# Performance work log

Hardware: AMD Instinct MI355X
Metric: run time of the kernel (lower is better)

Reference implementation:

```python
import jax, jax.numpy as jnp
import numpy as np

V = 780        # junction-tree vocab size
N = 50000      # total nodes in batch
M = 100001     # total messages (+1 null slot at index 0)
K = 6          # padded max neighbors
H = 256        # hidden size
B = 64         # number of trees (scope entries)
DEPTH = 6      # GRU depth


def setup_inputs() -> dict:
    key = jax.random.key(0)
    ks = jax.random.split(key, 12)
    p = lambda k, s: jax.random.normal(k, s, jnp.float32) * 0.02
    return {
        "fnode": jax.random.randint(ks[0], (N,), 0, V),
        "fmess": jax.random.randint(ks[1], (M,), 0, N),
        "node_graph": jax.random.randint(ks[2], (N, K), 0, M),
        "mess_graph": jax.random.randint(ks[3], (M, K), 0, M),
        "scope_st": jax.random.randint(ks[4], (B,), 0, N),
        "emb": p(ks[5], (V, H)),
        "Wz": p(ks[6], (H, 2 * H)), "bz": jnp.zeros((H,), jnp.float32),
        "Wr": p(ks[7], (H, H)),
        "Ur": p(ks[8], (H, H)), "bu": jnp.zeros((H,), jnp.float32),
        "Wh": p(ks[9], (H, 2 * H)), "bh": jnp.zeros((H,), jnp.float32),
        "Wo": p(ks[10], (H, 2 * H)), "bo": jnp.zeros((H,), jnp.float32),
    }


def reference(fnode, fmess, node_graph, mess_graph, scope_st,
              emb, Wz, bz, Wr, Ur, bu, Wh, bh, Wo, bo):
    fnode_e = emb[fnode]                       # [N, H] embedded node features
    x = fnode_e[fmess]                         # [M, H] per-message source features
    mask = jnp.ones((M, 1), jnp.float32).at[0].set(0.0)  # zero the null message
    # W_r(x) depends only on x; hoist it out of the loop (same math as original)
    xWr = (x @ Wr.T)[:, None, :]               # [M, 1, H]

    h = jnp.zeros((M, H), jnp.float32)
    for _ in range(DEPTH):
        h_nei = h[mess_graph]                  # [M, K, H] gather neighbor messages
        sum_h = h_nei.sum(axis=1)              # [M, H]
        z = jax.nn.sigmoid(jnp.concatenate([x, sum_h], axis=1) @ Wz.T + bz)
        r = jax.nn.sigmoid(xWr + h_nei @ Ur.T + bu)   # [M, K, H]
        sum_gated_h = (r * h_nei).sum(axis=1)  # [M, H]
        pre_h = jnp.tanh(jnp.concatenate([x, sum_gated_h], axis=1) @ Wh.T + bh)
        h = ((1.0 - z) * sum_h + z * pre_h) * mask

    mess_nei = h[node_graph].sum(axis=1)       # [N, H]
    node_vecs = jax.nn.relu(
        jnp.concatenate([fnode_e, mess_nei], axis=-1) @ Wo.T + bo)  # [N, H]
    tree_vecs = node_vecs[scope_st]            # [B, H] root vector per tree
    return tree_vecs, h
```

## Files before the change

### kernel.cpp

```cpp
#include <hip/hip_runtime.h>

typedef unsigned short u16;
typedef unsigned int   u32;
typedef short bf16x8 __attribute__((ext_vector_type(8)));
typedef float f32x4  __attribute__((ext_vector_type(4)));

#define V_ 780
#define N_ 50000
#define M_ 100001
#define K_ 6
#define H_ 256
#define B_ 64
#define DEPTH_ 6

#define HE_LD 512

typedef __attribute__((address_space(3))) u32 lds_u32;
typedef __attribute__((address_space(1))) const u32 glb_u32;
__device__ __forceinline__ void dma16(const void* g, void* l){
  __builtin_amdgcn_global_load_lds((glb_u32*)g, (lds_u32*)l, 16, 0, 0);
}

__device__ __forceinline__ float b2f(u16 u){
  union { u32 i; float f; } x; x.i = ((u32)u) << 16; return x.f;
}
__device__ __forceinline__ u16 f2b(float f){
  union { float f; u32 i; } x; x.f = f;
  u32 r = x.i + 0x7fffu + ((x.i >> 16) & 1u);
  return (u16)(r >> 16);
}
__device__ __forceinline__ float rcp_(float x){ return __builtin_amdgcn_rcpf(x); }
__device__ __forceinline__ float sigm(float x){ return rcp_(1.f + __expf(-x)); }
__device__ __forceinline__ float tanh_(float x){
  x = fminf(fmaxf(x, -15.f), 15.f);
  float e = __expf(2.f*x);
  return (e - 1.f) * rcp_(e + 1.f);
}
__device__ __forceinline__ int swz(int r){ return (r + (r >> 2)) & 3; }

__global__ void k_tables(const float* __restrict__ emb,
    const float* __restrict__ Wz, const float* __restrict__ bz,
    const float* __restrict__ Wr, const float* __restrict__ bu,
    const float* __restrict__ Wh, const float* __restrict__ bh,
    const float* __restrict__ Wo, const float* __restrict__ bo,
    float* __restrict__ tWz, float* __restrict__ tXr,
    float* __restrict__ tWh, float* __restrict__ tWo){
  int v = blockIdx.x, q = blockIdx.y, j = threadIdx.x;
  __shared__ float e[H_];
  e[j] = emb[v*H_ + j];
  __syncthreads();
  const float* w; const float* b; float* o; int ld;
  if      (q == 0){ w = Wz; b = bz; o = tWz; ld = 2*H_; }
  else if (q == 1){ w = Wr; b = bu; o = tXr; ld = H_;   }
  else if (q == 2){ w = Wh; b = bh; o = tWh; ld = 2*H_; }
  else            { w = Wo; b = bo; o = tWo; ld = 2*H_; }
  const float* wr = w + (size_t)j*ld;
  float a0 = 0.f, a1 = 0.f;
  #pragma unroll 4
  for (int i = 0; i < H_; i += 8){
    float4 x = *(const float4*)(wr + i);
    float4 y = *(const float4*)(wr + i + 4);
    a0 += e[i  ]*x.x + e[i+1]*x.y + e[i+2]*x.z + e[i+3]*x.w;
    a1 += e[i+4]*y.x + e[i+5]*y.y + e[i+6]*y.z + e[i+7]*y.w;
  }
  float val = a0 + a1 + b[j];
  if (q == 1) val = __expf(-val);
  o[v*H_ + j] = val;
}

__global__ void k_convw(const float* __restrict__ Ur, const float* __restrict__ Wz,
                        const float* __restrict__ Wh,
                        u16* __restrict__ Urb, u16* __restrict__ Wzb, u16* __restrict__ Whb){
  int r = blockIdx.x, j = threadIdx.x;
  Urb[r*H_ + j] = f2b(Ur[r*H_ + j]);
  Wzb[r*H_ + j] = f2b(Wz[r*(2*H_) + H_ + j]);
  Whb[r*H_ + j] = f2b(Wh[r*(2*H_) + H_ + j]);
}

__global__ void k_init(const int* __restrict__ fnode, const int* __restrict__ fmess,
                       const float* __restrict__ tWz, const float* __restrict__ tWh,
                       int* __restrict__ vmsg, u16* __restrict__ hE){
  int m = blockIdx.x, j = threadIdx.x;
  int v = fnode[fmess[m]];
  if (j == 0) vmsg[m] = v;
  float val = (m == 0) ? 0.f : sigm(tWz[v*H_ + j])*tanh_(tWh[v*H_ + j]);
  hE[(size_t)m*HE_LD + j] = f2b(val);
}

__global__ void k_gather(const u16* __restrict__ hE,
                         const int* __restrict__ mg, const int* __restrict__ vmsg,
                         const float* __restrict__ tXr,
                         u16* __restrict__ sumh, u16* __restrict__ sumg){
  int m = blockIdx.x*4 + (threadIdx.x >> 6);
  if (m >= M_) return;
  const int lane = threadIdx.x & 63;
  int v = vmsg[m];
  float4 X = *(const float4*)(tXr + (size_t)v*H_ + lane*4);
  const int2* mgp = (const int2*)(mg + m*K_);
  int2 g01 = mgp[0], g23 = mgp[1], g45 = mgp[2];
  int gs[K_] = {g01.x, g01.y, g23.x, g23.y, g45.x, g45.y};
  const char* bc = (const char*)hE;
  const u32 cb = (u32)lane * 8u;
  float s0=0.f,s1=0.f,s2=0.f,s3=0.f, a0=0.f,a1=0.f,a2=0.f,a3=0.f;
  #pragma unroll
  for (int k=0;k<K_;k++){
    u32 off = ((u32)gs[k] << 10) + cb;
    uint2 hp = *(const uint2*)(bc + off);
    uint2 ep = *(const uint2*)(bc + off + 512);
    float h0=b2f((u16)hp.x), h1=b2f((u16)(hp.x>>16));
    float h2=b2f((u16)hp.y), h3=b2f((u16)(hp.y>>16));
    float e0=b2f((u16)ep.x), e1=b2f((u16)(ep.x>>16));
    float e2=b2f((u16)ep.y), e3=b2f((u16)(ep.y>>16));
    s0+=h0; s1+=h1; s2+=h2; s3+=h3;
    a0 += rcp_(fmaf(X.x,e0,1.f))*h0;
    a1 += rcp_(fmaf(X.y,e1,1.f))*h1;
    a2 += rcp_(fmaf(X.z,e2,1.f))*h2;
    a3 += rcp_(fmaf(X.w,e3,1.f))*h3;
  }
  uint2 sh, sg;
  sh.x = (u32)f2b(s0) | ((u32)f2b(s1)<<16);
  sh.y = (u32)f2b(s2) | ((u32)f2b(s3)<<16);
  sg.x = (u32)f2b(a0) | ((u32)f2b(a1)<<16);
  sg.y = (u32)f2b(a2) | ((u32)f2b(a3)<<16);
  *(uint2*)((char*)sumh + ((size_t)m<<9) + cb) = sh;
  *(uint2*)((char*)sumg + ((size_t)m<<9) + cb) = sg;
}

__global__ __launch_bounds__(512,4) void k_gemmE(
    const u16* hE, const u16* __restrict__ W){
  __shared__ __align__(16) u16 lA[128*32];
  __shared__ __align__(16) u16 lB[256*32];
  const int t    = threadIdx.x;
  const int m0   = blockIdx.x * 128;
  const int lane = t & 63, wave = t >> 6;
  const int wrow = wave >> 2, wcol = wave & 3;
  const int l16  = lane & 15, kc8 = lane >> 4;

  const int rA = t >> 2, cA = t & 3;
  const int kA = (cA ^ swz(rA)) * 8;
  const int gmA = (m0 + rA < M_) ? (m0 + rA) : (M_ - 1);
  u16* const dA = lA + (size_t)(wave*64)*8;
  int rB[2], kB[2];
  u16* dB[2];
  #pragma unroll
  for (int p=0;p<2;p++){
    int s = t + 512*p;
    rB[p] = s >> 2; int cB = s & 3;
    kB[p] = (cB ^ swz(rB[p])) * 8;
    dB[p] = lB + (size_t)(wave*64 + 512*p)*8;
  }

  f32x4 acc[4][4];
  #pragma unroll
  for (int r=0;r<4;r++)
    #pragma unroll
    for (int c=0;c<4;c++)
      #pragma unroll
      for (int q=0;q<4;q++) acc[r][c][q] = 0.f;

  for (int k0=0; k0<H_; k0+=32){
    __syncthreads();
    dma16(hE + (size_t)gmA*HE_LD + k0 + kA, dA);
    #pragma unroll
    for (int p=0;p<2;p++)
      dma16(W + (size_t)rB[p]*H_ + k0 + kB[p], dB[p]);
    __syncthreads();
    bf16x8 aF[4], bF[4];
    #pragma unroll
    for (int r=0;r<4;r++){
      int row = wrow*64 + r*16 + l16;
      aF[r] = *(const bf16x8*)(&lA[row*32 + ((kc8 ^ swz(row))*8)]);
    }
    #pragma unroll
    for (int c=0;c<4;c++){
      int row = wcol*64 + c*16 + l16;
      bF[c] = *(const bf16x8*)(&lB[row*32 + ((kc8 ^ swz(row))*8)]);
    }
    #pragma unroll
    for (int r=0;r<4;r++)
      #pragma unroll
      for (int c=0;c<4;c++)
        acc[r][c] = __builtin_amdgcn_mfma_f32_16x16x32_bf16(aF[r], bF[c], acc[r][c], 0,0,0);
  }

  u16* C = (u16*)hE;
  #pragma unroll
  for (int r=0;r<4;r++){
    #pragma unroll
    for (int c=0;c<4;c++){
      int mb = m0 + wrow*64 + r*16 + kc8*4;
      int n  = wcol*64 + c*16 + l16;
      #pragma unroll
      for (int q=0;q<4;q++){
        int m = mb + q;
        if (m < M_) C[(size_t)m*HE_LD + H_ + n] = f2b(__expf(-acc[r][c][q]));
      }
    }
  }
}

template<bool FIN>
__global__ __launch_bounds__(512,4) void k_gemmzh(
    const u16* __restrict__ sumh, const u16* __restrict__ sumg,
    const u16* __restrict__ Wzb, const u16* __restrict__ Whb,
    const float* __restrict__ tWz, const float* __restrict__ tWh,
    const int* __restrict__ vmsg,
    u16* __restrict__ dst, float* __restrict__ hf){
  __shared__ __align__(16) u16 lH[128*32];
  __shared__ __align__(16) u16 lG[128*32];
  __shared__ __align__(16) u16 lZ[128*32];
  __shared__ __align__(16) u16 lW[128*32];
  const int t    = threadIdx.x;
  const int m0   = (blockIdx.x >> 1) * 128;
  const int n0   = (blockIdx.x & 1) * 128;
  const int lane = t & 63, wave = t >> 6;
  const int wrow = wave >> 1, wcol = wave & 1;
  const int l16  = lane & 15, kc8 = lane >> 4;

  const int rS = t >> 2, cS = t & 3;
  const int kS = (cS ^ swz(rS)) * 8;
  const int gmS = (m0 + rS < M_) ? (m0 + rS) : (M_ - 1);
  const int gnS = n0 + rS;
  const int dOff = (wave*64)*8;

  f32x4 accZ[2][4], accH[2][4];
  #pragma unroll
  for (int r=0;r<2;r++)
    #pragma unroll
    for (int c=0;c<4;c++)
      #pragma unroll
      for (int q=0;q<4;q++){ accZ[r][c][q]=0.f; accH[r][c][q]=0.f; }

  for (int k0=0; k0<H_; k0+=32){
    __syncthreads();
    dma16(sumh + (size_t)gmS*H_ + k0 + kS, lH + dOff);
    dma16(sumg + (size_t)gmS*H_ + k0 + kS, lG + dOff);
    dma16(Wzb  + (size_t)gnS*H_ + k0 + kS, lZ + dOff);
    dma16(Whb  + (size_t)gnS*H_ + k0 + kS, lW + dOff);
    __syncthreads();
    bf16x8 aH[2], aG[2];
    #pragma unroll
    for (int r=0;r<2;r++){
      int row = wrow*32 + r*16 + l16;
      int ao = row*32 + ((kc8 ^ swz(row))*8);
      aH[r] = *(const bf16x8*)&lH[ao];
      aG[r] = *(const bf16x8*)&lG[ao];
    }
    #pragma unroll
    for (int c=0;c<4;c++){
      int row = wcol*64 + c*16 + l16;
      int bo = row*32 + ((kc8 ^ swz(row))*8);
      bf16x8 bZ = *(const bf16x8*)&lZ[bo];
      bf16x8 bW = *(const bf16x8*)&lW[bo];
      #pragma unroll
      for (int r=0;r<2;r++){
        accZ[r][c] = __builtin_amdgcn_mfma_f32_16x16x32_bf16(aH[r], bZ, accZ[r][c], 0,0,0);
        accH[r][c] = __builtin_amdgcn_mfma_f32_16x16x32_bf16(aG[r], bW, accH[r][c], 0,0,0);
      }
    }
  }

  #pragma unroll
  for (int r=0;r<2;r++){
    #pragma unroll
    for (int q=0;q<4;q++){
      int m  = m0 + wrow*32 + r*16 + kc8*4 + q;
      int mr = (m < M_) ? m : (M_ - 1);
      int v  = vmsg[mr];
      #pragma unroll
      for (int c=0;c<4;c++){
        int n = n0 + wcol*64 + c*16 + l16;
        float z   = sigm(tWz[v*H_ + n] + accZ[r][c][q]);
        float pre = tanh_(tWh[v*H_ + n] + accH[r][c][q]);
        float sh  = b2f(sumh[(size_t)mr*H_ + n]);
        float o   = (m == 0) ? 0.f : (1.f - z)*sh + z*pre;
        if (m < M_){
          if (FIN) hf[(size_t)m*H_ + n] = o;
          else     dst[(size_t)m*HE_LD + n] = f2b(o);
        }
      }
    }
  }
}

__global__ void k_final(const float* __restrict__ h, const int* __restrict__ ng,
                        const int* __restrict__ fnode, const int* __restrict__ scope,
                        const float* __restrict__ tWo, const float* __restrict__ Wo,
                        float* __restrict__ out){
  int b = blockIdx.x, j = threadIdx.x;
  int n = scope[b];
  __shared__ float mn[H_];
  float s = 0.f;
  #pragma unroll
  for (int k=0;k<K_;k++){
    int g = ng[n*K_ + k];
    s += h[(size_t)g*H_ + j];
  }
  mn[j] = s;
  __syncthreads();
  int v = fnode[n];
  float acc = tWo[v*H_ + j];
  const float* w = Wo + j*(2*H_) + H_;
  for (int i=0;i<H_;i+=4){
    float4 a = *(const float4*)(w+i);
    acc += mn[i]*a.x + mn[i+1]*a.y + mn[i+2]*a.z + mn[i+3]*a.w;
  }
  out[b*H_ + j] = fmaxf(acc, 0.f);
}

__global__ void k_zero(float* __restrict__ out, int n){
  int i = blockIdx.x*256 + threadIdx.x;
  int stride = gridDim.x*256;
  for (; i < n; i += stride) out[i] = 0.f;
}

extern "C" void kernel_launch(void* const* d_in, const int* in_sizes, int n_in,
                              void* d_out, int out_size, void* d_ws, size_t ws_size,
                              hipStream_t stream){
  const int* fnode      = (const int*)d_in[0];
  const int* fmess      = (const int*)d_in[1];
  const int* node_graph = (const int*)d_in[2];
  const int* mess_graph = (const int*)d_in[3];
  const int* scope_st   = (const int*)d_in[4];
  const float* emb = (const float*)d_in[5];
  const float* Wz  = (const float*)d_in[6];
  const float* bz  = (const float*)d_in[7];
  const float* Wr  = (const float*)d_in[8];
  const float* Ur  = (const float*)d_in[9];
  const float* bu  = (const float*)d_in[10];
  const float* Wh  = (const float*)d_in[11];
  const float* bh  = (const float*)d_in[12];
  const float* Wo  = (const float*)d_in[13];
  const float* bo  = (const float*)d_in[14];

  char* ws = (char*)d_ws;
  size_t off = 0;
  float* tWz = (float*)(ws + off); off += (size_t)V_*H_*4;
  float* tXr = (float*)(ws + off); off += (size_t)V_*H_*4;
  float* tWh = (float*)(ws + off); off += (size_t)V_*H_*4;
  float* tWo = (float*)(ws + off); off += (size_t)V_*H_*4;
  u16* Urb  = (u16*)(ws + off); off += (size_t)H_*H_*2;
  u16* Wzb  = (u16*)(ws + off); off += (size_t)H_*H_*2;
  u16* Whb  = (u16*)(ws + off); off += (size_t)H_*H_*2;
  int* vmsg = (int*)(ws + off); off += ((size_t)M_*4 + 1023) & ~(size_t)1023;
  u16* sumh = (u16*)(ws + off); off += (size_t)M_*H_*2;
  u16* sumg = (u16*)(ws + off); off += (size_t)M_*H_*2;

  if (ws_size < off){
    k_zero<<<2048, 256, 0, stream>>>((float*)d_out, out_size);
    return;
  }

  float* out = (float*)d_out;
  float* h   = out + (size_t)B_*H_;
  u16* hE = (u16*)h;

  const int MT128 = (M_ + 127)/128;
  const int GG    = 2*MT128;
  const int GB    = (M_ + 3)/4;

  k_tables<<<dim3(V_,4), H_, 0, stream>>>(emb, Wz, bz, Wr, bu, Wh, bh, Wo, bo,
                                          tWz, tXr, tWh, tWo);
  k_convw<<<H_, H_, 0, stream>>>(Ur, Wz, Wh, Urb, Wzb, Whb);
  k_init<<<M_, H_, 0, stream>>>(fnode, fmess, tWz, tWh, vmsg, hE);
  k_gemmE<<<MT128, 512, 0, stream>>>(hE, Urb);

  for (int it = 0; it < DEPTH_-1; ++it){
    k_gather<<<GB, 256, 0, stream>>>(hE, mess_graph, vmsg, tXr, sumh, sumg);
    if (it < DEPTH_-2){
      k_gemmzh<false><<<GG, 512, 0, stream>>>(sumh, sumg, Wzb, Whb,
                                              tWz, tWh, vmsg, hE, h);
      k_gemmE<<<MT128, 512, 0, stream>>>(hE, Urb);
    } else {
      k_gemmzh<true ><<<GG, 512, 0, stream>>>(sumh, sumg, Wzb, Whb,
                                              tWz, tWh, vmsg, hE, h);
    }
  }

  k_final<<<B_, H_, 0, stream>>>(h, node_graph, fnode, scope_st, tWo, Wo, out);
}
```

Measured before the change: 1.313 ms.

## Double-buffer LDS tiles in GEMM kernels and use nontemporal store for gated sums

The k_gemmE and k_gemmzh main loops now use two LDS buffers. The next K-slice is issued via global_load_lds while MFMAs run on the current slice, which cuts one of the two barriers per iteration. The gated-sum store in the gather kernel becomes a nontemporal store. LDS use per block doubles, which may cut occupancy under the launch bounds of 4 blocks per SM. The nontemporal hint may also hurt if the sumg data is read back soon from cache.

```diff
diff --git a/kernel.cpp b/kernel.cpp
--- a/kernel.cpp
+++ b/kernel.cpp
@@ -4,6 +4,7 @@
 typedef unsigned int   u32;
 typedef short bf16x8 __attribute__((ext_vector_type(8)));
 typedef float f32x4  __attribute__((ext_vector_type(4)));
+typedef u32   u32x2  __attribute__((ext_vector_type(2)));
 
 #define V_ 780
 #define N_ 50000
@@ -117,19 +118,20 @@
     a2 += rcp_(fmaf(X.z,e2,1.f))*h2;
     a3 += rcp_(fmaf(X.w,e3,1.f))*h3;
   }
-  uint2 sh, sg;
+  uint2 sh;
+  u32x2 sg;
   sh.x = (u32)f2b(s0) | ((u32)f2b(s1)<<16);
   sh.y = (u32)f2b(s2) | ((u32)f2b(s3)<<16);
-  sg.x = (u32)f2b(a0) | ((u32)f2b(a1)<<16);
-  sg.y = (u32)f2b(a2) | ((u32)f2b(a3)<<16);
+  sg[0] = (u32)f2b(a0) | ((u32)f2b(a1)<<16);
+  sg[1] = (u32)f2b(a2) | ((u32)f2b(a3)<<16);
   *(uint2*)((char*)sumh + ((size_t)m<<9) + cb) = sh;
-  *(uint2*)((char*)sumg + ((size_t)m<<9) + cb) = sg;
+  __builtin_nontemporal_store(sg, (u32x2*)((char*)sumg + ((size_t)m<<9) + cb));
 }
 
 __global__ __launch_bounds__(512,4) void k_gemmE(
     const u16* hE, const u16* __restrict__ W){
-  __shared__ __align__(16) u16 lA[128*32];
-  __shared__ __align__(16) u16 lB[256*32];
+  __shared__ __align__(16) u16 lA[2][128*32];
+  __shared__ __align__(16) u16 lB[2][256*32];
   const int t    = threadIdx.x;
   const int m0   = blockIdx.x * 128;
   const int lane = t & 63, wave = t >> 6;
@@ -139,15 +141,14 @@
   const int rA = t >> 2, cA = t & 3;
   const int kA = (cA ^ swz(rA)) * 8;
   const int gmA = (m0 + rA < M_) ? (m0 + rA) : (M_ - 1);
-  u16* const dA = lA + (size_t)(wave*64)*8;
-  int rB[2], kB[2];
-  u16* dB[2];
+  const int aOff = (wave*64)*8;
+  int rB[2], kB[2], bOff[2];
   #pragma unroll
   for (int p=0;p<2;p++){
     int s = t + 512*p;
     rB[p] = s >> 2; int cB = s & 3;
     kB[p] = (cB ^ swz(rB[p])) * 8;
-    dB[p] = lB + (size_t)(wave*64 + 512*p)*8;
+    bOff[p] = (wave*64 + 512*p)*8;
   }
 
   f32x4 acc[4][4];
@@ -158,29 +159,36 @@
       #pragma unroll
       for (int q=0;q<4;q++) acc[r][c][q] = 0.f;
 
-  for (int k0=0; k0<H_; k0+=32){
-    __syncthreads();
-    dma16(hE + (size_t)gmA*HE_LD + k0 + kA, dA);
+  auto stage = [&](int buf, int k0){
+    dma16(hE + (size_t)gmA*HE_LD + k0 + kA, &lA[buf][aOff]);
     #pragma unroll
     for (int p=0;p<2;p++)
-      dma16(W + (size_t)rB[p]*H_ + k0 + kB[p], dB[p]);
-    __syncthreads();
+      dma16(W + (size_t)rB[p]*H_ + k0 + kB[p], &lB[buf][bOff[p]]);
+  };
+
+  stage(0, 0);
+  __syncthreads();
+  int cur = 0;
+  for (int ks = 0; ks < 8; ++ks){
+    if (ks < 7) stage(cur^1, (ks+1)*32);
     bf16x8 aF[4], bF[4];
     #pragma unroll
     for (int r=0;r<4;r++){
       int row = wrow*64 + r*16 + l16;
-      aF[r] = *(const bf16x8*)(&lA[row*32 + ((kc8 ^ swz(row))*8)]);
+      aF[r] = *(const bf16x8*)(&lA[cur][row*32 + ((kc8 ^ swz(row))*8)]);
     }
     #pragma unroll
     for (int c=0;c<4;c++){
       int row = wcol*64 + c*16 + l16;
-      bF[c] = *(const bf16x8*)(&lB[row*32 + ((kc8 ^ swz(row))*8)]);
+      bF[c] = *(const bf16x8*)(&lB[cur][row*32 + ((kc8 ^ swz(row))*8)]);
     }
     #pragma unroll
     for (int r=0;r<4;r++)
       #pragma unroll
       for (int c=0;c<4;c++)
         acc[r][c] = __builtin_amdgcn_mfma_f32_16x16x32_bf16(aF[r], bF[c], acc[r][c], 0,0,0);
+    if (ks < 7) __syncthreads();
+    cur ^= 1;
   }
 
   u16* C = (u16*)hE;
@@ -206,10 +214,10 @@
     const float* __restrict__ tWz, const float* __restrict__ tWh,
     const int* __restrict__ vmsg,
     u16* __restrict__ dst, float* __restrict__ hf){
-  __shared__ __align__(16) u16 lH[128*32];
-  __shared__ __align__(16) u16 lG[128*32];
-  __shared__ __align__(16) u16 lZ[128*32];
-  __shared__ __align__(16) u16 lW[128*32];
+  __shared__ __align__(16) u16 lH[2][128*32];
+  __shared__ __align__(16) u16 lG[2][128*32];
+  __shared__ __align__(16) u16 lZ[2][128*32];
+  __shared__ __align__(16) u16 lW[2][128*32];
   const int t    = threadIdx.x;
   const int m0   = (blockIdx.x >> 1) * 128;
   const int n0   = (blockIdx.x & 1) * 128;
@@ -231,33 +239,40 @@
       #pragma unroll
       for (int q=0;q<4;q++){ accZ[r][c][q]=0.f; accH[r][c][q]=0.f; }
 
-  for (int k0=0; k0<H_; k0+=32){
-    __syncthreads();
-    dma16(sumh + (size_t)gmS*H_ + k0 + kS, lH + dOff);
-    dma16(sumg + (size_t)gmS*H_ + k0 + kS, lG + dOff);
-    dma16(Wzb  + (size_t)gnS*H_ + k0 + kS, lZ + dOff);
-    dma16(Whb  + (size_t)gnS*H_ + k0 + kS, lW + dOff);
-    __syncthreads();
+  auto stage = [&](int buf, int k0){
+    dma16(sumh + (size_t)gmS*H_ + k0 + kS, &lH[buf][dOff]);
+    dma16(sumg + (size_t)gmS*H_ + k0 + kS, &lG[buf][dOff]);
+    dma16(Wzb  + (size_t)gnS*H_ + k0 + kS, &lZ[buf][dOff]);
+    dma16(Whb  + (size_t)gnS*H_ + k0 + kS, &lW[buf][dOff]);
+  };
+
+  stage(0, 0);
+  __syncthreads();
+  int cur = 0;
+  for (int ks = 0; ks < 8; ++ks){
+    if (ks < 7) stage(cur^1, (ks+1)*32);
     bf16x8 aH[2], aG[2];
     #pragma unroll
     for (int r=0;r<2;r++){
       int row = wrow*32 + r*16 + l16;
       int ao = row*32 + ((kc8 ^ swz(row))*8);
-      aH[r] = *(const bf16x8*)&lH[ao];
-      aG[r] = *(const bf16x8*)&lG[ao];
+      aH[r] = *(const bf16x8*)&lH[cur][ao];
+      aG[r] = *(const bf16x8*)&lG[cur][ao];
     }
     #pragma unroll
     for (int c=0;c<4;c++){
       int row = wcol*64 + c*16 + l16;
       int bo = row*32 + ((kc8 ^ swz(row))*8);
-      bf16x8 bZ = *(const bf16x8*)&lZ[bo];
-      bf16x8 bW = *(const bf16x8*)&lW[bo];
+      bf16x8 bZ = *(const bf16x8*)&lZ[cur][bo];
+      bf16x8 bW = *(const bf16x8*)&lW[cur][bo];
       #pragma unroll
       for (int r=0;r<2;r++){
         accZ[r][c] = __builtin_amdgcn_mfma_f32_16x16x32_bf16(aH[r], bZ, accZ[r][c], 0,0,0);
         accH[r][c] = __builtin_amdgcn_mfma_f32_16x16x32_bf16(aG[r], bW, accH[r][c], 0,0,0);
       }
     }
+    if (ks < 7) __syncthreads();
+    cur ^= 1;
   }
 
   #pragma unroll
```

After: 1.353 ms. +3.0%, slower.

## Retile gate GEMM to 64-row by full-256-column blocks and nontemporal-store sumg

Applied to the files above, without the earlier changes.

The z/h gate GEMM kernel now gives each block 64 message rows across all 256 output columns, where it used to give 128 rows by 128 columns. Each sumh/sumg row tile is therefore read from global memory once instead of twice, while the bf16 weight tiles (Wz, Wh) are loaded in full per block and are likely cache-resident. The gather kernel also writes sumg with a nontemporal store to reduce cache pollution. The trade-off is more blocks, more weight traffic per block and a larger LDS footprint. The nontemporal hint could also hurt, because the next kernel reads sumg right away.

```diff
diff --git a/kernel.cpp b/kernel.cpp
--- a/kernel.cpp
+++ b/kernel.cpp
@@ -4,6 +4,7 @@
 typedef unsigned int   u32;
 typedef short bf16x8 __attribute__((ext_vector_type(8)));
 typedef float f32x4  __attribute__((ext_vector_type(4)));
+typedef u32   u32x2  __attribute__((ext_vector_type(2)));
 
 #define V_ 780
 #define N_ 50000
@@ -117,13 +118,14 @@
     a2 += rcp_(fmaf(X.z,e2,1.f))*h2;
     a3 += rcp_(fmaf(X.w,e3,1.f))*h3;
   }
-  uint2 sh, sg;
+  uint2 sh;
+  u32x2 sg;
   sh.x = (u32)f2b(s0) | ((u32)f2b(s1)<<16);
   sh.y = (u32)f2b(s2) | ((u32)f2b(s3)<<16);
-  sg.x = (u32)f2b(a0) | ((u32)f2b(a1)<<16);
-  sg.y = (u32)f2b(a2) | ((u32)f2b(a3)<<16);
+  sg[0] = (u32)f2b(a0) | ((u32)f2b(a1)<<16);
+  sg[1] = (u32)f2b(a2) | ((u32)f2b(a3)<<16);
   *(uint2*)((char*)sumh + ((size_t)m<<9) + cb) = sh;
-  *(uint2*)((char*)sumg + ((size_t)m<<9) + cb) = sg;
+  __builtin_nontemporal_store(sg, (u32x2*)((char*)sumg + ((size_t)m<<9) + cb));
 }
 
 __global__ __launch_bounds__(512,4) void k_gemmE(
@@ -206,22 +208,30 @@
     const float* __restrict__ tWz, const float* __restrict__ tWh,
     const int* __restrict__ vmsg,
     u16* __restrict__ dst, float* __restrict__ hf){
-  __shared__ __align__(16) u16 lH[128*32];
-  __shared__ __align__(16) u16 lG[128*32];
-  __shared__ __align__(16) u16 lZ[128*32];
-  __shared__ __align__(16) u16 lW[128*32];
+  __shared__ __align__(16) u16 lH[64*32];
+  __shared__ __align__(16) u16 lG[64*32];
+  __shared__ __align__(16) u16 lZ[256*32];
+  __shared__ __align__(16) u16 lW[256*32];
   const int t    = threadIdx.x;
-  const int m0   = (blockIdx.x >> 1) * 128;
-  const int n0   = (blockIdx.x & 1) * 128;
+  const int m0   = blockIdx.x * 64;
   const int lane = t & 63, wave = t >> 6;
-  const int wrow = wave >> 1, wcol = wave & 1;
+  const int wrow = wave >> 2, wcol = wave & 3;
   const int l16  = lane & 15, kc8 = lane >> 4;
 
-  const int rS = t >> 2, cS = t & 3;
-  const int kS = (cS ^ swz(rS)) * 8;
-  const int gmS = (m0 + rS < M_) ? (m0 + rS) : (M_ - 1);
-  const int gnS = n0 + rS;
-  const int dOff = (wave*64)*8;
+  const int matA = t >> 8;
+  const int tmA  = t & 255;
+  const int rS   = tmA >> 2, cS = tmA & 3;
+  const int kS   = (cS ^ swz(rS)) * 8;
+  const int gmS  = (m0 + rS < M_) ? (m0 + rS) : (M_ - 1);
+  const u16* srcA = matA ? sumg : sumh;
+  u16* const dA   = (matA ? lG : lH) + ((wave & 3) * 64) * 8;
+
+  const int rB0 = t >> 2, rB1 = rB0 + 128;
+  const int kB  = ((t & 3) ^ swz(rB0)) * 8;
+  u16* const dZ0 = lZ + (wave*64)*8;
+  u16* const dZ1 = lZ + (wave*64 + 512)*8;
+  u16* const dW0 = lW + (wave*64)*8;
+  u16* const dW1 = lW + (wave*64 + 512)*8;
 
   f32x4 accZ[2][4], accH[2][4];
   #pragma unroll
@@ -233,10 +243,11 @@
 
   for (int k0=0; k0<H_; k0+=32){
     __syncthreads();
-    dma16(sumh + (size_t)gmS*H_ + k0 + kS, lH + dOff);
-    dma16(sumg + (size_t)gmS*H_ + k0 + kS, lG + dOff);
-    dma16(Wzb  + (size_t)gnS*H_ + k0 + kS, lZ + dOff);
-    dma16(Whb  + (size_t)gnS*H_ + k0 + kS, lW + dOff);
+    dma16(srcA + (size_t)gmS*H_ + k0 + kS, dA);
+    dma16(Wzb + (size_t)rB0*H_ + k0 + kB, dZ0);
+    dma16(Wzb + (size_t)rB1*H_ + k0 + kB, dZ1);
+    dma16(Whb + (size_t)rB0*H_ + k0 + kB, dW0);
+    dma16(Whb + (size_t)rB1*H_ + k0 + kB, dW1);
     __syncthreads();
     bf16x8 aH[2], aG[2];
     #pragma unroll
@@ -269,7 +280,7 @@
       int v  = vmsg[mr];
       #pragma unroll
       for (int c=0;c<4;c++){
-        int n = n0 + wcol*64 + c*16 + l16;
+        int n = wcol*64 + c*16 + l16;
         float z   = sigm(tWz[v*H_ + n] + accZ[r][c][q]);
         float pre = tanh_(tWh[v*H_ + n] + accH[r][c][q]);
         float sh  = b2f(sumh[(size_t)mr*H_ + n]);
@@ -356,7 +367,7 @@
   u16* hE = (u16*)h;
 
   const int MT128 = (M_ + 127)/128;
-  const int GG    = 2*MT128;
+  const int MT64  = (M_ + 63)/64;
   const int GB    = (M_ + 3)/4;
 
   k_tables<<<dim3(V_,4), H_, 0, stream>>>(emb, Wz, bz, Wr, bu, Wh, bh, Wo, bo,
@@ -368,12 +379,12 @@
   for (int it = 0; it < DEPTH_-1; ++it){
     k_gather<<<GB, 256, 0, stream>>>(hE, mess_graph, vmsg, tXr, sumh, sumg);
     if (it < DEPTH_-2){
-      k_gemmzh<false><<<GG, 512, 0, stream>>>(sumh, sumg, Wzb, Whb,
-                                              tWz, tWh, vmsg, hE, h);
+      k_gemmzh<false><<<MT64, 512, 0, stream>>>(sumh, sumg, Wzb, Whb,
+                                                tWz, tWh, vmsg, hE, h);
       k_gemmE<<<MT128, 512, 0, stream>>>(hE, Urb);
     } else {
-      k_gemmzh<true ><<<GG, 512, 0, stream>>>(sumh, sumg, Wzb, Whb,
-                                              tWz, tWh, vmsg, hE, h);
+      k_gemmzh<true ><<<MT64, 512, 0, stream>>>(sumh, sumg, Wzb, Whb,
+                                                tWz, tWh, vmsg, hE, h);
     }
   }
 
```

Result: slower. 1.377 ms (+4.9%).
